# Kernel tuning notes

Measured on AMD Instinct MI355X. Metric: run time of the kernel, lower is better.

Reference implementation:

```python
import jax, jax.numpy as jnp
import numpy as np

ALPHA = 0.2  # LeakyReLU negative slope


def gat_layer(x, W, a, alpha=ALPHA):
    """Multi-head dense GAT layer.
    x: (B, N, F); W: (H, F, O); a: (H, 2*O, 1).
    Returns (B, N, H*O) — ELU(head outputs) concatenated over heads.
    """
    H, F, O = W.shape
    Wh = jnp.einsum('bnf,hfo->bhno', x, W)          # (B,H,N,O)
    a_src = a[:, :O, 0]                              # (H,O)
    a_dst = a[:, O:, 0]                              # (H,O)
    s_src = jnp.einsum('bhno,ho->bhn', Wh, a_src)    # (B,H,N)
    s_dst = jnp.einsum('bhno,ho->bhn', Wh, a_dst)    # (B,H,N)
    e = s_src[..., :, None] + s_dst[..., None, :]    # (B,H,N,N)
    e = jax.nn.leaky_relu(e, negative_slope=alpha)
    att = jax.nn.softmax(e, axis=-1)                 # softmax over neighbors j
    out = jnp.einsum('bhnm,bhmo->bhno', att, Wh)     # (B,H,N,O)
    out = jax.nn.elu(out)
    B, _, N, _ = out.shape
    return jnp.transpose(out, (0, 2, 1, 3)).reshape(B, N, H * O)


def setup_inputs() -> dict:
    key = jax.random.key(0)
    ks = jax.random.split(key, 5)
    B, N = 32, 1024
    x = jax.random.normal(ks[0], (B, N, 4), dtype=jnp.float32)
    # layer1: nfeat=4, nhid=2, nheads=3
    W1 = jax.random.normal(ks[1], (3, 4, 2), dtype=jnp.float32) * 0.5
    a1 = jax.random.normal(ks[2], (3, 4, 1), dtype=jnp.float32) * 0.5
    # layer2: nfeat=6, nhid=4, nheads=1
    W2 = jax.random.normal(ks[3], (1, 6, 4), dtype=jnp.float32) * 0.5
    a2 = jax.random.normal(ks[4], (1, 8, 1), dtype=jnp.float32) * 0.5
    return {"x": x, "W1": W1, "a1": a1, "W2": W2, "a2": a2}


def reference(x, W1, a1, W2, a2):
    h = gat_layer(x, W1, a1)   # (B, N, 6)
    y = gat_layer(h, W2, a2)   # (B, N, 4)
    return y
```

## Files before the change

kernel.cpp:

```cpp
#include <hip/hip_runtime.h>


#define GAT_ALPHA 0.2f
#define LOG2E 1.44269504088896f

typedef float v2f __attribute__((ext_vector_type(2)));

template <int F, int O, int H, int RPB>
__global__ __launch_bounds__(256) void gat_layer_kernel(
    const float* __restrict__ x,
    const float* __restrict__ Wt,
    const float* __restrict__ at,
    float* __restrict__ out)
{
    constexpr int N = 1024, NT = 256, S = 16;
    constexpr int NP = N / 2;
    constexpr int R = RPB / 16;
    constexpr int Q = O + 1;
    constexpr int CHUNKS = N / RPB;
    constexpr int PAD = R * Q + 1;

    const int bid   = blockIdx.x;
    const int chunk = bid % CHUNKS;
    const int h     = (bid / CHUNKS) % H;
    const int b     = bid / (CHUNKS * H);
    const int tid   = threadIdx.x;
    const int wv    = tid >> 6, l = tid & 63;
    const int r     = (l >> 2) & 15;
    const int sq    = l & 3;
    const int s     = (wv << 2) | sq;

    float Wl[F][O];
#pragma unroll
    for (int f = 0; f < F; ++f)
#pragma unroll
        for (int o = 0; o < O; ++o) Wl[f][o] = Wt[(h * F + f) * O + o];
    float asrc[O], adst[O];
#pragma unroll
    for (int o = 0; o < O; ++o) {
        asrc[o] = at[h * 2 * O + o];
        adst[o] = at[h * 2 * O + O + o];
    }

    __shared__ float4 sE[NP];
    __shared__ float4 sW01[NP];
    __shared__ float4 sW23[(O > 2) ? NP : 1];
    __shared__ float  sredu[4 * 16 * PAD];

    const float* xb = x + (size_t)b * N * F;
#pragma unroll
    for (int qq = 0; qq < NP / NT; ++qq) {
        const int q = qq * NT + tid;
        float xv[2][F];
        if constexpr (F == 4) {
            const float4 va = ((const float4*)xb)[2 * q];
            const float4 vb = ((const float4*)xb)[2 * q + 1];
            xv[0][0] = va.x; xv[0][1] = va.y; xv[0][2] = va.z; xv[0][3] = va.w;
            xv[1][0] = vb.x; xv[1][1] = vb.y; xv[1][2] = vb.z; xv[1][3] = vb.w;
        } else {
            const float4* x4 = (const float4*)xb;
            const float2* x2 = (const float2*)xb;
            const float4 fa = x4[3 * q];
            const float2 fb = x2[6 * q + 2];
            const float2 fc = x2[6 * q + 3];
            const float4 fd = x4[3 * q + 2];
            xv[0][0] = fa.x; xv[0][1] = fa.y; xv[0][2] = fa.z; xv[0][3] = fa.w;
            xv[0][4] = fb.x; xv[0][5] = fb.y;
            xv[1][0] = fc.x; xv[1][1] = fc.y;
            xv[1][2] = fd.x; xv[1][3] = fd.y; xv[1][4] = fd.z; xv[1][5] = fd.w;
        }
        float wh[2][O], d[2];
#pragma unroll
        for (int p = 0; p < 2; ++p) {
            d[p] = 0.0f;
#pragma unroll
            for (int o = 0; o < O; ++o) {
                float acc = 0.0f;
#pragma unroll
                for (int f = 0; f < F; ++f) acc += xv[p][f] * Wl[f][o];
                wh[p][o] = acc; d[p] += acc * adst[o];
            }
        }
        const float t0 = d[0] * LOG2E, t1 = d[1] * LOG2E;
        sE[q] = make_float4(__builtin_amdgcn_exp2f(t0),
                            __builtin_amdgcn_exp2f(t1),
                            __builtin_amdgcn_exp2f(GAT_ALPHA * t0),
                            __builtin_amdgcn_exp2f(GAT_ALPHA * t1));
        sW01[q] = make_float4(wh[0][0], wh[1][0], wh[0][1], wh[1][1]);
        if constexpr (O > 2)
            sW23[q] = make_float4(wh[0][2], wh[1][2], wh[0][3], wh[1][3]);
    }
    __syncthreads();

    float rho[R];
#pragma unroll
    for (int j = 0; j < R; ++j) {
        const int row = chunk * RPB + r + 16 * j;
        const int qr = row >> 1, cp = row & 1;
        const float4 w01 = sW01[qr];
        float sn = (cp ? w01.y : w01.x) * asrc[0] + (cp ? w01.w : w01.z) * asrc[1];
        if constexpr (O > 2) {
            const float4 w23 = sW23[qr];
            sn += (cp ? w23.y : w23.x) * asrc[2] + (cp ? w23.w : w23.z) * asrc[3];
        }
        rho[j] = __builtin_amdgcn_exp2f(0.8f * LOG2E * sn);
    }

    v2f den[R], num[R][O];
#pragma unroll
    for (int j = 0; j < R; ++j) {
        den[j] = (v2f)(0.0f);
#pragma unroll
        for (int o = 0; o < O; ++o) num[j][o] = (v2f)(0.0f);
    }

#pragma unroll 4
    for (int p = 0; p < NP / S; ++p) {
        const int q = p * S + s;
        const float4 e4 = sE[q];
        const float4 w4 = sW01[q];
        const v2f E1 = {e4.x, e4.y}, E2 = {e4.z, e4.w};
        const v2f W0 = {w4.x, w4.y}, W1v = {w4.z, w4.w};
        v2f W2v, W3v;
        if constexpr (O > 2) {
            const float4 w4b = sW23[q];
            W2v = (v2f){w4b.x, w4b.y}; W3v = (v2f){w4b.z, w4b.w};
        }
#pragma unroll
        for (int j = 0; j < R; ++j) {
            const v2f t = rho[j] * E1;
            v2f w;
            w.x = fmaxf(t.x, E2.x);
            w.y = fmaxf(t.y, E2.y);
            den[j] += w;
            num[j][0] += w * W0;
            num[j][1] += w * W1v;
            if constexpr (O > 2) {
                num[j][2] += w * W2v;
                num[j][3] += w * W3v;
            }
        }
    }

#pragma unroll
    for (int j = 0; j < R; ++j) {
        float dn = den[j].x + den[j].y;
        dn += __shfl_xor(dn, 1, 64);
        dn += __shfl_xor(dn, 2, 64);
        float nm[O];
#pragma unroll
        for (int o = 0; o < O; ++o) {
            nm[o] = num[j][o].x + num[j][o].y;
            nm[o] += __shfl_xor(nm[o], 1, 64);
            nm[o] += __shfl_xor(nm[o], 2, 64);
        }
        if (sq == 0) {
            const int base = (wv * 16 + r) * PAD + j * Q;
            sredu[base] = dn;
#pragma unroll
            for (int o = 0; o < O; ++o) sredu[base + 1 + o] = nm[o];
        }
    }
    __syncthreads();

    for (int idx = tid; idx < RPB * O; idx += NT) {
        const int rowl = idx / O, o = idx % O;
        const int rr = rowl & 15, jj = rowl >> 4;
        float dn = 0.0f, nm = 0.0f;
#pragma unroll
        for (int ww = 0; ww < 4; ++ww) {
            const int base = (ww * 16 + rr) * PAD + jj * Q;
            dn += sredu[base];
            nm += sredu[base + 1 + o];
        }
        float v = nm / dn;
        v = (v > 0.0f) ? v : (__expf(v) - 1.0f);
        const int row = chunk * RPB + rowl;
        out[((size_t)b * N + row) * (H * O) + h * O + o] = v;
    }
}

extern "C" void kernel_launch(void* const* d_in, const int* in_sizes, int n_in,
                              void* d_out, int out_size, void* d_ws, size_t ws_size,
                              hipStream_t stream) {
    const float* x  = (const float*)d_in[0];
    const float* W1 = (const float*)d_in[1];
    const float* a1 = (const float*)d_in[2];
    const float* W2 = (const float*)d_in[3];
    const float* a2 = (const float*)d_in[4];

    float* h1 = (float*)d_ws;
    float* y  = (float*)d_out;

    constexpr int B = 32;
    gat_layer_kernel<4, 2, 3, 64><<<B * 3 * 16, 256, 0, stream>>>(x, W1, a1, h1);
    gat_layer_kernel<6, 4, 1, 32><<<B * 1 * 32, 256, 0, stream>>>(h1, W2, a2, y);
}
```

Measured before the change: 82.06 us.

## Give each wavefront its own rows and reduce across lanes with shuffles

Each of the four wavefronts now owns a disjoint slice of rows. Sixteen lanes per row stride over the neighbor pairs and combine their partial sums with a full-wavefront xor-shuffle reduction, which removes the shared-memory reduction buffer, its second barrier and the cross-wave combine loop. The normalization and ELU epilogue runs in registers and writes vectorized float2 or float4 stores. The block index is reordered so batch varies fastest, and launch bounds gain a minimum-waves hint. The trade-off is more shuffle steps per row, with only lane group sl==0 doing the epilogue.

New measurement: 82.84 us. Within noise of the previous version (+1.0%).

```diff
diff --git a/kernel.cpp b/kernel.cpp
--- a/kernel.cpp
+++ b/kernel.cpp
@@ -6,29 +6,28 @@
 
 typedef float v2f __attribute__((ext_vector_type(2)));
 
-template <int F, int O, int H, int RPB>
-__global__ __launch_bounds__(256) void gat_layer_kernel(
+template <int F, int O, int H, int RPB, int MINW>
+__global__ __launch_bounds__(256, MINW) void gat_layer_kernel(
     const float* __restrict__ x,
     const float* __restrict__ Wt,
     const float* __restrict__ at,
     float* __restrict__ out)
 {
-    constexpr int N = 1024, NT = 256, S = 16;
+    constexpr int N = 1024, NT = 256;
     constexpr int NP = N / 2;
-    constexpr int R = RPB / 16;
-    constexpr int Q = O + 1;
+    constexpr int WROWS = RPB / 4;
+    constexpr int R = WROWS / 4;
     constexpr int CHUNKS = N / RPB;
-    constexpr int PAD = R * Q + 1;
 
     const int bid   = blockIdx.x;
-    const int chunk = bid % CHUNKS;
-    const int h     = (bid / CHUNKS) % H;
-    const int b     = bid / (CHUNKS * H);
+    const int b     = bid & 31;
+    const int rest  = bid >> 5;
+    const int h     = rest % H;
+    const int chunk = rest / H;
     const int tid   = threadIdx.x;
     const int wv    = tid >> 6, l = tid & 63;
-    const int r     = (l >> 2) & 15;
-    const int sq    = l & 3;
-    const int s     = (wv << 2) | sq;
+    const int sl    = l >> 2;
+    const int rg    = l & 3;
 
     float Wl[F][O];
 #pragma unroll
@@ -45,7 +44,6 @@
     __shared__ float4 sE[NP];
     __shared__ float4 sW01[NP];
     __shared__ float4 sW23[(O > 2) ? NP : 1];
-    __shared__ float  sredu[4 * 16 * PAD];
 
     const float* xb = x + (size_t)b * N * F;
 #pragma unroll
@@ -92,10 +90,11 @@
     }
     __syncthreads();
 
+    const int rowbase = chunk * RPB + wv * WROWS;
     float rho[R];
 #pragma unroll
     for (int j = 0; j < R; ++j) {
-        const int row = chunk * RPB + r + 16 * j;
+        const int row = rowbase + rg + 4 * j;
         const int qr = row >> 1, cp = row & 1;
         const float4 w01 = sW01[qr];
         float sn = (cp ? w01.y : w01.x) * asrc[0] + (cp ? w01.w : w01.z) * asrc[1];
@@ -115,8 +114,8 @@
     }
 
 #pragma unroll 4
-    for (int p = 0; p < NP / S; ++p) {
-        const int q = p * S + s;
+    for (int p = 0; p < NP / 16; ++p) {
+        const int q = p * 16 + sl;
         const float4 e4 = sE[q];
         const float4 w4 = sW01[q];
         const v2f E1 = {e4.x, e4.y}, E2 = {e4.z, e4.w};
@@ -145,38 +144,31 @@
 #pragma unroll
     for (int j = 0; j < R; ++j) {
         float dn = den[j].x + den[j].y;
-        dn += __shfl_xor(dn, 1, 64);
-        dn += __shfl_xor(dn, 2, 64);
         float nm[O];
 #pragma unroll
-        for (int o = 0; o < O; ++o) {
-            nm[o] = num[j][o].x + num[j][o].y;
-            nm[o] += __shfl_xor(nm[o], 1, 64);
-            nm[o] += __shfl_xor(nm[o], 2, 64);
+        for (int o = 0; o < O; ++o) nm[o] = num[j][o].x + num[j][o].y;
+#pragma unroll
+        for (int off = 4; off < 64; off <<= 1) {
+            dn += __shfl_xor(dn, off, 64);
+#pragma unroll
+            for (int o = 0; o < O; ++o) nm[o] += __shfl_xor(nm[o], off, 64);
         }
-        if (sq == 0) {
-            const int base = (wv * 16 + r) * PAD + j * Q;
-            sredu[base] = dn;
+        if (sl == 0) {
+            const float inv = 1.0f / dn;
+            float v[O];
 #pragma unroll
-            for (int o = 0; o < O; ++o) sredu[base + 1 + o] = nm[o];
+            for (int o = 0; o < O; ++o) {
+                const float t = nm[o] * inv;
+                v[o] = (t > 0.0f) ? t : (__expf(t) - 1.0f);
+            }
+            const int row = rowbase + rg + 4 * j;
+            float* po = out + ((size_t)b * N + row) * (H * O) + h * O;
+            if constexpr (O == 2) {
+                *(float2*)po = make_float2(v[0], v[1]);
+            } else {
+                *(float4*)po = make_float4(v[0], v[1], v[2], v[3]);
+            }
         }
-    }
-    __syncthreads();
-
-    for (int idx = tid; idx < RPB * O; idx += NT) {
-        const int rowl = idx / O, o = idx % O;
-        const int rr = rowl & 15, jj = rowl >> 4;
-        float dn = 0.0f, nm = 0.0f;
-#pragma unroll
-        for (int ww = 0; ww < 4; ++ww) {
-            const int base = (ww * 16 + rr) * PAD + jj * Q;
-            dn += sredu[base];
-            nm += sredu[base + 1 + o];
-        }
-        float v = nm / dn;
-        v = (v > 0.0f) ? v : (__expf(v) - 1.0f);
-        const int row = chunk * RPB + rowl;
-        out[((size_t)b * N + row) * (H * O) + h * O + o] = v;
     }
 }
 
@@ -193,6 +185,6 @@
     float* y  = (float*)d_out;
 
     constexpr int B = 32;
-    gat_layer_kernel<4, 2, 3, 64><<<B * 3 * 16, 256, 0, stream>>>(x, W1, a1, h1);
-    gat_layer_kernel<6, 4, 1, 32><<<B * 1 * 32, 256, 0, stream>>>(h1, W2, a2, y);
+    gat_layer_kernel<4, 2, 3, 64, 6><<<B * 3 * 16, 256, 0, stream>>>(x, W1, a1, h1);
+    gat_layer_kernel<6, 4, 1, 32, 4><<<B * 1 * 32, 256, 0, stream>>>(h1, W2, a2, y);
 }
```
